# Kernel optimization log

Hardware: AMD Instinct MI355X
Metric: run time of the kernel (lower is better)

## Reference

```python
import jax, jax.numpy as jnp
import numpy as np
from jax import lax

K_LOCAL = 8
CHUNK = 1024


def _local_features(template, surf_xyz, point_feat):
    # template: (B,T,3), surf_xyz: (B,S,3), point_feat: (B,S,D)
    B, T, _ = template.shape
    _, S, D = point_feat.shape
    n_chunks = T // CHUNK  # T chosen divisible by CHUNK
    tmpl = template.reshape(B, n_chunks, CHUNK, 3).transpose(1, 0, 2, 3)  # (n_chunks,B,c,3)
    s_sq = jnp.sum(surf_xyz * surf_xyz, axis=-1)  # (B,S)

    def body(carry, t):  # t: (B,c,3)
        t_sq = jnp.sum(t * t, axis=-1)  # (B,c)
        # squared distances; monotone in true distance so top-k indices match cdist
        d2 = t_sq[..., None] + s_sq[:, None, :] - 2.0 * jnp.einsum('bcd,bsd->bcs', t, surf_xyz)
        _, idx = lax.top_k(-d2, K_LOCAL)  # (B,c,k) nearest
        flat = idx.reshape(B, -1)  # (B,c*k)
        g = jnp.take_along_axis(point_feat, flat[..., None], axis=1)  # (B,c*k,D)
        local = g.reshape(B, CHUNK, K_LOCAL, D).mean(axis=2)  # (B,c,D)
        return carry, local

    _, locals_ = lax.scan(body, None, tmpl)  # (n_chunks,B,c,D)
    return locals_.transpose(1, 0, 2, 3).reshape(B, T, D)


def setup_inputs() -> dict:
    key = jax.random.key(0)
    ks = jax.random.split(key, 12)
    B, T, S, D, G = 4, 16384, 8192, 256, 512
    inp_dim, H = 3 + D + G, 256
    w = lambda k, sh: (jax.random.normal(k, sh, dtype=jnp.float32) * 0.02)
    return {
        'template': jax.random.normal(ks[0], (B, T, 3), dtype=jnp.float32),
        'surf_xyz': jax.random.normal(ks[1], (B, S, 3), dtype=jnp.float32),
        'global_feat': jax.random.normal(ks[2], (B, G), dtype=jnp.float32),
        'point_feat': jax.random.normal(ks[3], (B, S, D), dtype=jnp.float32),
        'dw1': w(ks[4], (inp_dim, H)), 'db1': jnp.zeros((H,), jnp.float32),
        'dw2': w(ks[5], (H, H)), 'db2': jnp.zeros((H,), jnp.float32),
        'dw3': w(ks[6], (H, 3)), 'db3': jnp.zeros((3,), jnp.float32),
        'mw1': w(ks[7], (inp_dim, H // 2)), 'mb1': jnp.zeros((H // 2,), jnp.float32),
        'mw2': w(ks[8], (H // 2, 64)), 'mb2': jnp.zeros((64,), jnp.float32),
        'mw3': w(ks[9], (64, 1)), 'mb3': jnp.zeros((1,), jnp.float32),
    }


def reference(template, surf_xyz, global_feat, point_feat,
              dw1, db1, dw2, db2, dw3, db3,
              mw1, mb1, mw2, mb2, mw3, mb3):
    B, T, _ = template.shape
    local = _local_features(template, surf_xyz, point_feat)  # (B,T,256)
    g = jnp.broadcast_to(global_feat[:, None, :], (B, T, global_feat.shape[-1]))
    x = jnp.concatenate([template, local, g], axis=-1)  # (B,T,771)
    # disp head (dropout = identity in eval)
    h = jax.nn.relu(x @ dw1 + db1)
    h = jax.nn.relu(h @ dw2 + db2)
    disp = h @ dw3 + db3  # (B,T,3)
    # material head
    m = jax.nn.relu(x @ mw1 + mb1)
    m = jax.nn.relu(m @ mw2 + mb2)
    mat = jax.nn.sigmoid(m @ mw3 + mb3)[..., 0]  # (B,T)
    return disp, mat
```

## Files before the change

kernel.cpp:

```cpp
#include <hip/hip_runtime.h>
#include <cstdint>


#define T_PTS 16384
#define S_PTS 8192
#define B_SZ 4
#define D_FEAT 256
#define G_FEAT 512
#define M_ROWS (B_SZ * T_PTS)
#define K1 320
#define N1 384
#define DISP_SZ (M_ROWS * 3)
#define NCHUNK 4
#define CHUNK_S (S_PTS / NCHUNK)
#define NCELL 32768

using u16 = unsigned short;
typedef short bf16x8 __attribute__((ext_vector_type(8)));
typedef float f32x4 __attribute__((ext_vector_type(4)));

__device__ __forceinline__ u16 f2bf(float f) {
  uint32_t x = __builtin_bit_cast(uint32_t, f);
  x += 0x7fffu + ((x >> 16) & 1u);
  return (u16)(x >> 16);
}
__device__ __forceinline__ float bf2f(u16 h) {
  uint32_t x = ((uint32_t)h) << 16;
  return __builtin_bit_cast(float, x);
}
__device__ __forceinline__ void gload16(void* lds, const void* g) {
  __builtin_amdgcn_global_load_lds(
      (const __attribute__((address_space(1))) unsigned int*)g,
      (__attribute__((address_space(3))) unsigned int*)lds, 16, 0, 0);
}


__global__ __launch_bounds__(256) void prep_surf(const float* __restrict__ sxyz,
                                                 float4* __restrict__ surfp) {
  int i = blockIdx.x * 256 + threadIdx.x;
  float x = sxyz[(size_t)i * 3], y = sxyz[(size_t)i * 3 + 1], z = sxyz[(size_t)i * 3 + 2];
  float4 v;
  v.x = x; v.y = y; v.z = z; v.w = fmaf(x, x, fmaf(y, y, z * z));
  surfp[i] = v;
}

__global__ __launch_bounds__(256) void prep_w(
    const float* __restrict__ dw1, const float* __restrict__ mw1,
    const float* __restrict__ dw2, const float* __restrict__ mw2,
    u16* __restrict__ w1t, u16* __restrict__ w2t, u16* __restrict__ w2bt) {
  int i = blockIdx.x * 256 + threadIdx.x;
  if (i < 122880) {
    int n = i / 320, k = i % 320;
    float v = 0.f;
    if (k < 256)      v = (n < 256) ? dw1[(size_t)(3 + k) * 256 + n] : mw1[(size_t)(3 + k) * 128 + (n - 256)];
    else if (k < 259) v = (n < 256) ? dw1[(size_t)(k - 256) * 256 + n] : mw1[(size_t)(k - 256) * 128 + (n - 256)];
    w1t[i] = f2bf(v);
  } else if (i < 188416) {
    int j = i - 122880;
    int n = j >> 8, k = j & 255;
    w2t[j] = f2bf(dw2[(size_t)k * 256 + n]);
  } else {
    int j = i - 188416;
    int n = j >> 7, k = j & 127;
    w2bt[j] = f2bf(mw2[(size_t)k * 64 + n]);
  }
}

__global__ __launch_bounds__(512) void bias1_k(
    const float* __restrict__ gf, const float* __restrict__ dw1,
    const float* __restrict__ mw1, const float* __restrict__ db1,
    const float* __restrict__ mb1, float* __restrict__ bias1) {
  __shared__ float red[512];
  int b = blockIdx.x, nc = blockIdx.y;
  int tn = threadIdx.x & 127, tk = threadIdx.x >> 7;
  int n = nc * 128 + tn;
  const float* g = gf + b * G_FEAT;
  float s = 0.f;
  if (n < 256) {
    for (int k = tk * 128; k < tk * 128 + 128; k++)
      s = fmaf(g[k], dw1[(size_t)(259 + k) * 256 + n], s);
  } else {
    for (int k = tk * 128; k < tk * 128 + 128; k++)
      s = fmaf(g[k], mw1[(size_t)(259 + k) * 128 + (n - 256)], s);
  }
  red[threadIdx.x] = s;
  __syncthreads();
  if (tk == 0) {
    float base = (n < 256) ? db1[n] : mb1[n - 256];
    bias1[b * N1 + n] = base + ((red[tn] + red[tn + 128]) + (red[tn + 256] + red[tn + 384]));
  }
}


__device__ __forceinline__ int spread5(int v) {
  return (v & 1) | ((v & 2) << 2) | ((v & 4) << 4) | ((v & 8) << 6) | ((v & 16) << 8);
}
__device__ __forceinline__ int morton15(float x, float y, float z) {
  int ix = (int)fminf(31.f, fmaxf(0.f, (x + 4.f) * 4.f));
  int iy = (int)fminf(31.f, fmaxf(0.f, (y + 4.f) * 4.f));
  int iz = (int)fminf(31.f, fmaxf(0.f, (z + 4.f) * 4.f));
  return (spread5(ix) << 2) | (spread5(iy) << 1) | spread5(iz);
}

__global__ __launch_bounds__(256) void zbins_k(int* __restrict__ bins) {
  bins[blockIdx.x * 256 + threadIdx.x] = 0;
}

__global__ __launch_bounds__(256) void hist_t_k(const float* __restrict__ tmpl,
                                                int* __restrict__ bins_t,
                                                int* __restrict__ cellb) {
  int i = blockIdx.x * 256 + threadIdx.x;
  int b = i >> 14;
  int c = morton15(tmpl[(size_t)i * 3], tmpl[(size_t)i * 3 + 1], tmpl[(size_t)i * 3 + 2]);
  cellb[i] = c;
  atomicAdd(&bins_t[b * NCELL + c], 1);
}

__global__ __launch_bounds__(1024) void scan_k(int* __restrict__ bins) {
  __shared__ int sd[2048];
  int* bb = bins + blockIdx.x * NCELL;
  int tid = threadIdx.x;
  int running = 0;
  for (int c = 0; c < NCELL / 1024; ++c) {
    int v = bb[c * 1024 + tid];
    sd[tid] = v;
    __syncthreads();
    int cur = 0;
#pragma unroll
    for (int s = 0; s < 10; ++s) {
      int off = 1 << s;
      int val = sd[cur * 1024 + tid] + ((tid >= off) ? sd[cur * 1024 + tid - off] : 0);
      sd[(1 - cur) * 1024 + tid] = val;
      __syncthreads();
      cur ^= 1;
    }
    int incl = sd[cur * 1024 + tid];
    bb[c * 1024 + tid] = running + incl - v;
    running += sd[cur * 1024 + 1023];
    __syncthreads();
  }
}

__global__ __launch_bounds__(256) void scatter_t_k(const float* __restrict__ tmpl,
                                                   const int* __restrict__ cellb,
                                                   int* __restrict__ bins_t,
                                                   int* __restrict__ perm,
                                                   float4* __restrict__ tmplS) {
  int i = blockIdx.x * 256 + threadIdx.x;
  int b = i >> 14, t = i & 16383;
  int pos = atomicAdd(&bins_t[b * NCELL + cellb[i]], 1);
  int dst = (b << 14) + pos;
  perm[dst] = t;
  float4 v;
  v.x = tmpl[(size_t)i * 3]; v.y = tmpl[(size_t)i * 3 + 1]; v.z = tmpl[(size_t)i * 3 + 2];
  v.w = 0.f;
  tmplS[dst] = v;
}

__global__ __launch_bounds__(256, 4) void knn_part_k(const float4* __restrict__ surfp,
                                                     const float4* __restrict__ tmplS,
                                                     float* __restrict__ part_d,
                                                     int* __restrict__ part_i) {
  __shared__ float4 sb[CHUNK_S];
  const int ch = blockIdx.y, b = blockIdx.z;
  const int t = (blockIdx.x << 8) + threadIdx.x;
  const int gi = b * T_PTS + t;

  const float4* sp = surfp + (size_t)b * S_PTS + ch * CHUNK_S;
#pragma unroll
  for (int i = 0; i < 8; i++)
    gload16((char*)sb + (size_t)(i * 256 + threadIdx.x) * 16, sp + i * 256 + threadIdx.x);

  float4 tp = tmplS[gi];
  float nx = -2.f * tp.x, ny = -2.f * tp.y, nz = -2.f * tp.z;
  float tsq = fmaf(tp.x, tp.x, fmaf(tp.y, tp.y, tp.z * tp.z));

  float dd[8]; int ii[8];
#pragma unroll
  for (int q = 0; q < 8; q++) { dd[q] = 3e38f; ii[q] = 0; }
  float worst = 3e38f;

  asm volatile("s_waitcnt vmcnt(0)" ::: "memory");
  __syncthreads();

  for (int g = 0; g < CHUNK_S / 8; ++g) {
    float4 c[8];
#pragma unroll
    for (int q = 0; q < 8; q++) c[q] = sb[g * 8 + q];
    float d2[8];
#pragma unroll
    for (int q = 0; q < 8; q++)
      d2[q] = fmaf(nx, c[q].x, fmaf(ny, c[q].y, fmaf(nz, c[q].z, tsq + c[q].w)));
    float m = fminf(fminf(fminf(d2[0], d2[1]), fminf(d2[2], d2[3])),
                    fminf(fminf(d2[4], d2[5]), fminf(d2[6], d2[7])));
    while (m < worst) {
      int qi = 7;
#pragma unroll
      for (int q = 6; q >= 0; --q) qi = (d2[q] == m) ? q : qi;
      int gx = g * 8 + qi;
#pragma unroll
      for (int r = 7; r >= 1; --r) {
        bool cr = m < dd[r], cr1 = m < dd[r - 1];
        dd[r] = cr ? (cr1 ? dd[r - 1] : m) : dd[r];
        ii[r] = cr ? (cr1 ? ii[r - 1] : gx) : ii[r];
      }
      bool c0 = m < dd[0];
      dd[0] = c0 ? m : dd[0];
      ii[0] = c0 ? gx : ii[0];
      worst = dd[7];
#pragma unroll
      for (int q = 0; q < 8; ++q) d2[q] = (q == qi) ? 3e38f : d2[q];
      m = fminf(fminf(fminf(d2[0], d2[1]), fminf(d2[2], d2[3])),
                fminf(fminf(d2[4], d2[5]), fminf(d2[6], d2[7])));
    }
  }

#pragma unroll
  for (int q = 0; q < 8; q++) {
    part_d[(size_t)(ch * 8 + q) * M_ROWS + gi] = dd[q];
    part_i[(size_t)(ch * 8 + q) * M_ROWS + gi] = ii[q] + ch * CHUNK_S;
  }
}

__global__ __launch_bounds__(256) void knn_merge_k(const float* __restrict__ part_d,
                                                   const int* __restrict__ part_i,
                                                   int* __restrict__ knn) {
  int pt = blockIdx.x * 256 + threadIdx.x;
  float d[32]; int x[32];
#pragma unroll
  for (int q = 0; q < 32; q++) {
    d[q] = part_d[(size_t)q * M_ROWS + pt];
    x[q] = part_i[(size_t)q * M_ROWS + pt];
  }
#pragma unroll
  for (int s = 0; s < 8; s++) {
    float bd = d[0]; int bx = x[0]; int bp = 0;
#pragma unroll
    for (int q = 1; q < 32; q++) {
      bool lt = (d[q] < bd) || (d[q] == bd && x[q] < bx);
      bd = lt ? d[q] : bd;
      bx = lt ? x[q] : bx;
      bp = lt ? q : bp;
    }
    knn[(size_t)pt * 8 + s] = bx;
#pragma unroll
    for (int q = 0; q < 32; q++)
      if (q == bp) d[q] = 3e38f;
  }
}

__global__ __launch_bounds__(256) void gather_k(const int* __restrict__ knn,
                                                const float* __restrict__ pf,
                                                const float4* __restrict__ tmplS,
                                                u16* __restrict__ xb) {
  int m = blockIdx.x * 4 + (threadIdx.x >> 6);
  int lane = threadIdx.x & 63;
  int b = m >> 14;
  const int* id = knn + (size_t)m * 8;
  const float* base = pf + (size_t)b * S_PTS * D_FEAT;
  float ax = 0, ay = 0, az = 0, aw = 0;
#pragma unroll
  for (int k = 0; k < 8; k++) {
    const float4* p = (const float4*)(base + (size_t)id[k] * D_FEAT) + lane;
    float4 v = *p;
    ax += v.x; ay += v.y; az += v.z; aw += v.w;
  }
  ushort4 o;
  o.x = f2bf(ax * 0.125f); o.y = f2bf(ay * 0.125f);
  o.z = f2bf(az * 0.125f); o.w = f2bf(aw * 0.125f);
  *(ushort4*)(xb + (size_t)m * K1 + lane * 4) = o;
  float4 tp = tmplS[m];
  float tv = (lane == 0) ? tp.x : (lane == 1) ? tp.y : (lane == 2) ? tp.z : 0.f;
  xb[(size_t)m * K1 + 256 + lane] = f2bf(tv);
}

template <int BM, int BN>
__global__ __launch_bounds__(256) void gemm_k(const u16* __restrict__ X, int ldx,
                                              const u16* __restrict__ Wt,
                                              const float* __restrict__ bias, int bstride,
                                              u16* __restrict__ Y, int ldy, int K) {
  constexpr int WM = 2, WN = 2;
  constexpr int FM = BM / WM / 16, FN = BN / WN / 16;
  __shared__ u16 As[BM * 64];
  __shared__ u16 Bs[BN * 64];
  const int tid = threadIdx.x, lane = tid & 63, wid = tid >> 6;
  const int m0 = blockIdx.x * BM, n0 = blockIdx.y * BN;
  const int wm0 = (wid / WN) * (BM / WM), wn0 = (wid % WN) * (BN / WN);

  f32x4 acc[FM][FN] = {};

  for (int kt = 0; kt < K; kt += 64) {
#pragma unroll
    for (int i = 0; i < BM * 8 / 256; i++) {
      int c = i * 256 + tid;
      int r = c >> 3, s = c & 7;
      int ss = s ^ (r & 7);
      gload16(As + c * 8, X + (size_t)(m0 + r) * ldx + kt + ss * 8);
    }
#pragma unroll
    for (int i = 0; i < BN * 8 / 256; i++) {
      int c = i * 256 + tid;
      int r = c >> 3, s = c & 7;
      int ss = s ^ (r & 7);
      gload16(Bs + c * 8, Wt + (size_t)(n0 + r) * K + kt + ss * 8);
    }
    __syncthreads();
#pragma unroll
    for (int kk = 0; kk < 2; kk++) {
      bf16x8 af[FM], bfr[FN];
#pragma unroll
      for (int i = 0; i < FM; i++) {
        int r = wm0 + i * 16 + (lane & 15);
        int q = kk * 4 + (lane >> 4);
        af[i] = *(const bf16x8*)(As + r * 64 + ((q ^ (r & 7)) * 8));
      }
#pragma unroll
      for (int j = 0; j < FN; j++) {
        int r = wn0 + j * 16 + (lane & 15);
        int q = kk * 4 + (lane >> 4);
        bfr[j] = *(const bf16x8*)(Bs + r * 64 + ((q ^ (r & 7)) * 8));
      }
#pragma unroll
      for (int i = 0; i < FM; i++)
#pragma unroll
        for (int j = 0; j < FN; j++)
          acc[i][j] = __builtin_amdgcn_mfma_f32_16x16x32_bf16(af[i], bfr[j], acc[i][j], 0, 0, 0);
    }
    __syncthreads();
  }

  const float* brow = bias + (size_t)(m0 / T_PTS) * bstride;
#pragma unroll
  for (int i = 0; i < FM; i++)
#pragma unroll
    for (int j = 0; j < FN; j++)
#pragma unroll
      for (int r = 0; r < 4; r++) {
        int rl = wm0 + i * 16 + (lane >> 4) * 4 + r;
        int cl = wn0 + j * 16 + (lane & 15);
        float v = acc[i][j][r] + brow[n0 + cl];
        v = fmaxf(v, 0.f);
        Y[(size_t)(m0 + rl) * ldy + n0 + cl] = f2bf(v);
      }
}

__global__ __launch_bounds__(256) void final_k(const u16* __restrict__ h2,
                                               const u16* __restrict__ m2,
                                               const float* __restrict__ dw3,
                                               const float* __restrict__ db3,
                                               const float* __restrict__ mw3,
                                               const float* __restrict__ mb3,
                                               const int* __restrict__ perm,
                                               float* __restrict__ out) {
  int m = blockIdx.x * 4 + (threadIdx.x >> 6);
  int lane = threadIdx.x & 63;
  ushort4 hv = *(const ushort4*)(h2 + (size_t)m * 256 + lane * 4);
  float hq[4] = {bf2f(hv.x), bf2f(hv.y), bf2f(hv.z), bf2f(hv.w)};
  float a0 = 0, a1 = 0, a2 = 0, am = 0;
#pragma unroll
  for (int q = 0; q < 4; q++) {
    int k = lane * 4 + q;
    a0 = fmaf(hq[q], dw3[(size_t)k * 3 + 0], a0);
    a1 = fmaf(hq[q], dw3[(size_t)k * 3 + 1], a1);
    a2 = fmaf(hq[q], dw3[(size_t)k * 3 + 2], a2);
  }
  if (lane < 16) {
    ushort4 mv = *(const ushort4*)(m2 + (size_t)m * 64 + lane * 4);
    float mq[4] = {bf2f(mv.x), bf2f(mv.y), bf2f(mv.z), bf2f(mv.w)};
#pragma unroll
    for (int q = 0; q < 4; q++) am = fmaf(mq[q], mw3[lane * 4 + q], am);
  }
#pragma unroll
  for (int off = 32; off > 0; off >>= 1) {
    a0 += __shfl_down(a0, off);
    a1 += __shfl_down(a1, off);
    a2 += __shfl_down(a2, off);
    am += __shfl_down(am, off);
  }
  if (lane == 0) {
    int b = m >> 14;
    int orig = (b << 14) + perm[m];
    out[(size_t)orig * 3 + 0] = a0 + db3[0];
    out[(size_t)orig * 3 + 1] = a1 + db3[1];
    out[(size_t)orig * 3 + 2] = a2 + db3[2];
    float s = am + mb3[0];
    out[DISP_SZ + orig] = 1.f / (1.f + expf(-s));
  }
}


extern "C" void kernel_launch(void* const* d_in, const int* in_sizes, int n_in,
                              void* d_out, int out_size, void* d_ws, size_t ws_size,
                              hipStream_t stream) {
  const float* tmpl = (const float*)d_in[0];
  const float* sxyz = (const float*)d_in[1];
  const float* gf   = (const float*)d_in[2];
  const float* pf   = (const float*)d_in[3];
  const float* dw1  = (const float*)d_in[4];
  const float* db1  = (const float*)d_in[5];
  const float* dw2  = (const float*)d_in[6];
  const float* db2  = (const float*)d_in[7];
  const float* dw3  = (const float*)d_in[8];
  const float* db3  = (const float*)d_in[9];
  const float* mw1  = (const float*)d_in[10];
  const float* mb1  = (const float*)d_in[11];
  const float* mw2  = (const float*)d_in[12];
  const float* mb2  = (const float*)d_in[13];
  const float* mw3  = (const float*)d_in[14];
  const float* mb3  = (const float*)d_in[15];

  char* ws = (char*)d_ws;
  float4* surfp  = (float4*)(ws + 0);
  int*    knn    = (int*)(ws + 524288);
  u16*    xb     = (u16*)(ws + 2621440);
  float*  part_d = (float*)(ws + 2621440);
  int*    part_i = (int*)(ws + 11010048);
  u16*    w1t    = (u16*)(ws + 44564480);
  u16*    w2t    = (u16*)(ws + 44810240);
  u16*    w2bt   = (u16*)(ws + 44941312);
  float*  bias1  = (float*)(ws + 44957696);
  u16*    h1     = (u16*)(ws + 44963840);
  int*    cellb  = (int*)(ws + 44963840);
  int*    bins   = (int*)(ws + 45225984);
  float4* tmplS  = (float4*)(ws + 45750272);
  u16*    h2     = (u16*)(ws + 95295488);
  u16*    m2     = (u16*)(ws + 128849920);
  int*    perm   = (int*)(ws + 137238528);
  float*  out    = (float*)d_out;

  prep_surf<<<128, 256, 0, stream>>>(sxyz, surfp);
  prep_w<<<768, 256, 0, stream>>>(dw1, mw1, dw2, mw2, w1t, w2t, w2bt);
  bias1_k<<<dim3(B_SZ, 3), 512, 0, stream>>>(gf, dw1, mw1, db1, mb1, bias1);
  zbins_k<<<512, 256, 0, stream>>>(bins);
  hist_t_k<<<256, 256, 0, stream>>>(tmpl, bins, cellb);
  scan_k<<<B_SZ, 1024, 0, stream>>>(bins);
  scatter_t_k<<<256, 256, 0, stream>>>(tmpl, cellb, bins, perm, tmplS);
  knn_part_k<<<dim3(64, NCHUNK, B_SZ), 256, 0, stream>>>(surfp, tmplS, part_d, part_i);
  knn_merge_k<<<256, 256, 0, stream>>>(part_d, part_i, knn);
  gather_k<<<16384, 256, 0, stream>>>(knn, pf, tmplS, xb);
  gemm_k<128, 128><<<dim3(512, 3), 256, 0, stream>>>(xb, K1, w1t, bias1, N1, h1, N1, K1);
  gemm_k<128, 128><<<dim3(512, 2), 256, 0, stream>>>(h1, N1, w2t, db2, 0, h2, 256, 256);
  gemm_k<128, 64><<<dim3(512, 1), 256, 0, stream>>>(h1 + 256, N1, w2bt, mb2, 0, m2, 64, 128);
  final_k<<<16384, 256, 0, stream>>>(h2, m2, dw3, db3, mw3, mb3, perm, out);
}
```

Measured before the change: 505.6 us.

## Stream surface points from global memory with register double-buffering in kNN

The brute-force kNN partial kernel no longer stages a surface chunk in LDS. Each thread now reads surface points directly from global memory (wave-uniform addresses, so they broadcast through cache), and register double-buffering overlaps the next group's loads with the current top-k update. The surface is split into 2 chunks instead of 4, so each thread scans more points but the merge kernel reads only 16 partial planes instead of 32. The risks are less parallelism in the partial kernel and global/scalar load latency replacing LDS reads.

```diff
diff --git a/kernel.cpp b/kernel.cpp
--- a/kernel.cpp
+++ b/kernel.cpp
@@ -11,8 +11,9 @@
 #define K1 320
 #define N1 384
 #define DISP_SZ (M_ROWS * 3)
-#define NCHUNK 4
+#define NCHUNK 2
 #define CHUNK_S (S_PTS / NCHUNK)
+#define NPLANE (NCHUNK * 8)
 #define NCELL 32768
 
 using u16 = unsigned short;
@@ -157,19 +158,15 @@
   tmplS[dst] = v;
 }
 
-__global__ __launch_bounds__(256, 4) void knn_part_k(const float4* __restrict__ surfp,
-                                                     const float4* __restrict__ tmplS,
-                                                     float* __restrict__ part_d,
-                                                     int* __restrict__ part_i) {
-  __shared__ float4 sb[CHUNK_S];
+__global__ __launch_bounds__(256) void knn_part_k(const float4* __restrict__ surfp,
+                                                  const float4* __restrict__ tmplS,
+                                                  float* __restrict__ part_d,
+                                                  int* __restrict__ part_i) {
   const int ch = blockIdx.y, b = blockIdx.z;
   const int t = (blockIdx.x << 8) + threadIdx.x;
   const int gi = b * T_PTS + t;
 
   const float4* sp = surfp + (size_t)b * S_PTS + ch * CHUNK_S;
-#pragma unroll
-  for (int i = 0; i < 8; i++)
-    gload16((char*)sb + (size_t)(i * 256 + threadIdx.x) * 16, sp + i * 256 + threadIdx.x);
 
   float4 tp = tmplS[gi];
   float nx = -2.f * tp.x, ny = -2.f * tp.y, nz = -2.f * tp.z;
@@ -180,13 +177,7 @@
   for (int q = 0; q < 8; q++) { dd[q] = 3e38f; ii[q] = 0; }
   float worst = 3e38f;
 
-  asm volatile("s_waitcnt vmcnt(0)" ::: "memory");
-  __syncthreads();
-
-  for (int g = 0; g < CHUNK_S / 8; ++g) {
-    float4 c[8];
-#pragma unroll
-    for (int q = 0; q < 8; q++) c[q] = sb[g * 8 + q];
+  auto proc = [&](const float4* c, int base) {
     float d2[8];
 #pragma unroll
     for (int q = 0; q < 8; q++)
@@ -197,7 +188,7 @@
       int qi = 7;
 #pragma unroll
       for (int q = 6; q >= 0; --q) qi = (d2[q] == m) ? q : qi;
-      int gx = g * 8 + qi;
+      int gx = base + qi;
 #pragma unroll
       for (int r = 7; r >= 1; --r) {
         bool cr = m < dd[r], cr1 = m < dd[r - 1];
@@ -213,6 +204,20 @@
       m = fminf(fminf(fminf(d2[0], d2[1]), fminf(d2[2], d2[3])),
                 fminf(fminf(d2[4], d2[5]), fminf(d2[6], d2[7])));
     }
+  };
+
+  float4 ca[8], cb[8];
+#pragma unroll
+  for (int q = 0; q < 8; q++) ca[q] = sp[q];
+
+  constexpr int NG = CHUNK_S / 8;
+  for (int g = 0; g < NG; g += 2) {
+#pragma unroll
+    for (int q = 0; q < 8; q++) cb[q] = sp[(g + 1) * 8 + q];
+    proc(ca, g * 8);
+#pragma unroll
+    for (int q = 0; q < 8; q++) ca[q] = sp[((g + 2) & (NG - 1)) * 8 + q];
+    proc(cb, (g + 1) * 8);
   }
 
 #pragma unroll
@@ -226,9 +231,9 @@
                                                    const int* __restrict__ part_i,
                                                    int* __restrict__ knn) {
   int pt = blockIdx.x * 256 + threadIdx.x;
-  float d[32]; int x[32];
-#pragma unroll
-  for (int q = 0; q < 32; q++) {
+  float d[NPLANE]; int x[NPLANE];
+#pragma unroll
+  for (int q = 0; q < NPLANE; q++) {
     d[q] = part_d[(size_t)q * M_ROWS + pt];
     x[q] = part_i[(size_t)q * M_ROWS + pt];
   }
@@ -236,7 +241,7 @@
   for (int s = 0; s < 8; s++) {
     float bd = d[0]; int bx = x[0]; int bp = 0;
 #pragma unroll
-    for (int q = 1; q < 32; q++) {
+    for (int q = 1; q < NPLANE; q++) {
       bool lt = (d[q] < bd) || (d[q] == bd && x[q] < bx);
       bd = lt ? d[q] : bd;
       bx = lt ? x[q] : bx;
@@ -244,7 +249,7 @@
     }
     knn[(size_t)pt * 8 + s] = bx;
 #pragma unroll
-    for (int q = 0; q < 32; q++)
+    for (int q = 0; q < NPLANE; q++)
       if (q == bp) d[q] = 3e38f;
   }
 }
```

Measured after the change: 518.3 us. 2.5% more time.
